# Kernel optimization log

Hardware: AMD Instinct MI355X
Metric: run time of the kernel (lower is better)

Reference implementation:

```python
import jax, jax.numpy as jnp
import numpy as np

ALPHA = 0.2          # LeakyReLU negative slope
NEG_INF = -9e15      # matches torch's -9000000000000000.0 mask value


def _gat_layer(x, adj_mask, W, a1, a2, concat):
    """One GraphAttentionLayerBatch (eval mode, dropout off).

    The original builds a_input = [h_i || h_j] of shape [B,N,N,2F] and dots
    with a = [a1; a2]; that is mathematically the separable score
    a1.h_i + a2.h_j, which we compute directly without the O(N^2*2F) tensor.
    """
    h = jnp.einsum('bnf,fo->bno', x, W)            # [B, N, F_out]
    f1 = jnp.einsum('bno,o->bn', h, a1)            # a1 . h_i
    f2 = jnp.einsum('bno,o->bn', h, a2)            # a2 . h_j
    e = jax.nn.leaky_relu(f1[:, :, None] + f2[:, None, :], negative_slope=ALPHA)
    e = jnp.where(adj_mask, e, NEG_INF)            # [B, N, N]
    att = jax.nn.softmax(e, axis=2)
    h_prime = jnp.einsum('bnm,bmo->bno', att, h)   # [B, N, F_out]
    return jax.nn.elu(h_prime) if concat else h_prime


def setup_inputs() -> dict:
    key = jax.random.key(0)
    ks = jax.random.split(key, 9)
    B, N, nfeat, nhid, nclass, H = 32, 512, 128, 64, 16, 8
    x = jax.random.normal(ks[0], (B, N, nfeat), dtype=jnp.float32)
    adj = jax.random.randint(ks[1], (B, N, N), 0, 2, dtype=jnp.int32)
    W_heads = jax.random.normal(ks[2], (H, nfeat, nhid), dtype=jnp.float32) * 0.1
    a1_heads = jax.random.normal(ks[3], (H, nhid), dtype=jnp.float32) * 0.1
    a2_heads = jax.random.normal(ks[4], (H, nhid), dtype=jnp.float32) * 0.1
    W_out = jax.random.normal(ks[5], (nhid * H, nclass), dtype=jnp.float32) * 0.05
    a1_out = jax.random.normal(ks[6], (nclass,), dtype=jnp.float32) * 0.1
    a2_out = jax.random.normal(ks[7], (nclass,), dtype=jnp.float32) * 0.1
    return {"x": x, "adj": adj, "W_heads": W_heads, "a1_heads": a1_heads,
            "a2_heads": a2_heads, "W_out": W_out, "a1_out": a1_out,
            "a2_out": a2_out}


def reference(x, adj, W_heads, a1_heads, a2_heads, W_out, a1_out, a2_out):
    mask = adj > 0  # [B, N, N]
    # multi-head attention layers (concat=True)
    heads = jax.vmap(lambda W, a1, a2: _gat_layer(x, mask, W, a1, a2, True))(
        W_heads, a1_heads, a2_heads)              # [H, B, N, nhid]
    H, B, N, F = heads.shape
    x_cat = jnp.transpose(heads, (1, 2, 0, 3)).reshape(B, N, H * F)
    # output attention layer (concat=False)
    return _gat_layer(x_cat, mask, W_out, a1_out, a2_out, False)
```

## Files before the change

### kernel.cpp

```cpp
#include <hip/hip_runtime.h>
#include <hip/hip_bf16.h>

#define GB 32
#define GN 512
#define GFIN 128
#define GFH 64
#define GH 8
#define GC 16

typedef short short8 __attribute__((ext_vector_type(8)));
typedef float f32x4 __attribute__((ext_vector_type(4)));

__device__ __forceinline__ ushort f2bf(float f) {
  unsigned u = __float_as_uint(f);
  return (ushort)((u + 0x7FFFu + ((u >> 16) & 1u)) >> 16);
}
__device__ __forceinline__ unsigned pk2(float a, float b) {
  float2 f2; f2.x = a; f2.y = b;
  __hip_bfloat162 h = __float22bfloat162_rn(f2);
  union { __hip_bfloat162 h; unsigned u; } cv;
  cv.h = h;
  return cv.u;
}
__device__ __forceinline__ short8 ones8() {
  short8 o;
#pragma unroll
  for (int i = 0; i < 8; ++i) o[i] = (short)0x3F80;
  return o;
}
__device__ __forceinline__ float fdiv_fast(float a, float b) {
  return a * __builtin_amdgcn_rcpf(b);
}

__global__ __launch_bounds__(256) void k_pack_gemm1(
    const int* __restrict__ adj, unsigned* __restrict__ mw,
    const float* __restrict__ xg, const float* __restrict__ Wg,
    const float* __restrict__ a1g, const float* __restrict__ a2g,
    ushort* __restrict__ VTg, float* __restrict__ f1g, float* __restrict__ f2g,
    const float* __restrict__ Wog, ushort* __restrict__ WoT) {
  __shared__ ushort Wt[64][136];
  __shared__ ushort xl[128][136];
  int blk = blockIdx.x;
  int tid = threadIdx.x;

  if (blk == 5120) {
    for (int i = tid; i < 512 * GC; i += 256) {
      int k = i & 511, cc = i >> 9;
      WoT[cc * 512 + k] = f2bf(Wog[(size_t)k * GC + cc]);
    }
    return;
  }
  if (blk >= 1024) {
    int pblk = blk - 1024;
    int lane = tid & 63;
    int base = pblk * 2048 + tid;
    int v[8];
#pragma unroll
    for (int it = 0; it < 8; ++it) v[it] = adj[(size_t)base + it * 256];
#pragma unroll
    for (int it = 0; it < 8; ++it) {
      unsigned long long m = __ballot(v[it] > 0);
      int idx = base + it * 256;
      if (lane == 0)       mw[idx >> 5] = (unsigned)m;
      else if (lane == 32) mw[idx >> 5] = (unsigned)(m >> 32);
    }
    return;
  }

  int bh = blk >> 2, rq = blk & 3;
  int b = bh >> 3, h = bh & 7;
  int r0 = rq * 128;
  int lane = tid & 63, w = tid >> 6;
  int c = lane & 15, q = lane >> 4;

  const float* Wh = Wg + (size_t)h * GFIN * GFH;
  for (int i = tid; i < GFIN * GFH; i += 256) {
    int f = i >> 6, j = i & 63;
    Wt[j][f] = f2bf(Wh[i]);
  }
  const float* xb = xg + ((size_t)b * GN + r0) * GFIN;
  for (int u = tid; u < 128 * 32; u += 256) {
    int row = u >> 5, c4 = u & 31;
    float4 xf = *(const float4*)&xb[(size_t)row * GFIN + c4 * 4];
    uint2 us;
    us.x = pk2(xf.x, xf.y);
    us.y = pk2(xf.z, xf.w);
    *(uint2*)&xl[row][c4 * 4] = us;
  }
  __syncthreads();

  short8 Bf[4][4];
#pragma unroll
  for (int cb = 0; cb < 4; ++cb)
#pragma unroll
    for (int kk = 0; kk < 4; ++kk)
      Bf[cb][kk] = *(const short8*)&Wt[cb * 16 + c][kk * 32 + q * 8];

  float a1v[4], a2v[4];
#pragma unroll
  for (int cb = 0; cb < 4; ++cb) {
    a1v[cb] = a1g[h * 64 + cb * 16 + c];
    a2v[cb] = a2g[h * 64 + cb * 16 + c];
  }

  f32x4 acc[2][4];
#pragma unroll
  for (int r = 0; r < 2; ++r)
#pragma unroll
    for (int cb = 0; cb < 4; ++cb) acc[r][cb] = (f32x4){0.f, 0.f, 0.f, 0.f};

#pragma unroll
  for (int kk = 0; kk < 4; ++kk) {
    short8 A0 = *(const short8*)&xl[(w * 2 + 0) * 16 + c][kk * 32 + q * 8];
    short8 A1 = *(const short8*)&xl[(w * 2 + 1) * 16 + c][kk * 32 + q * 8];
#pragma unroll
    for (int cb = 0; cb < 4; ++cb) {
      acc[0][cb] = __builtin_amdgcn_mfma_f32_16x16x32_bf16(A0, Bf[cb][kk], acc[0][cb], 0, 0, 0);
      acc[1][cb] = __builtin_amdgcn_mfma_f32_16x16x32_bf16(A1, Bf[cb][kk], acc[1][cb], 0, 0, 0);
    }
  }

  ushort* VT = VTg + (size_t)bh * GN * GFH;
  float* f1o = f1g + (size_t)bh * GN;
  float* f2o = f2g + (size_t)bh * GN;
#pragma unroll
  for (int rbi = 0; rbi < 2; ++rbi) {
    int rowb = r0 + (w * 2 + rbi) * 16 + q * 4;
    float v1[4] = {0.f, 0.f, 0.f, 0.f}, v2[4] = {0.f, 0.f, 0.f, 0.f};
#pragma unroll
    for (int cb = 0; cb < 4; ++cb) {
      f32x4 a = acc[rbi][cb];
      uint2 vs;
      vs.x = pk2(a[0], a[1]);
      vs.y = pk2(a[2], a[3]);
      *(uint2*)&VT[(size_t)(cb * 16 + c) * GN + rowb] = vs;
#pragma unroll
      for (int i = 0; i < 4; ++i) {
        v1[i] += a[i] * a1v[cb];
        v2[i] += a[i] * a2v[cb];
      }
    }
#pragma unroll
    for (int i = 0; i < 4; ++i) {
#pragma unroll
      for (int off = 1; off < 16; off <<= 1) {
        v1[i] += __shfl_xor(v1[i], off);
        v2[i] += __shfl_xor(v2[i], off);
      }
      if (c == 0) { f1o[rowb + i] = v1[i]; f2o[rowb + i] = v2[i]; }
    }
  }
}

__global__ __launch_bounds__(256, 4) void k_attn1(
    const ushort* __restrict__ VTg, const unsigned* __restrict__ mwg,
    const float* __restrict__ f1g, const float* __restrict__ f2g,
    ushort* __restrict__ xcb) {
  __shared__ ushort P[2][16][520];
  int blk = blockIdx.x;
  int bh = blk & 255, slice = blk >> 8;
  int b = bh >> 3, h = bh & 7;
  int r0 = slice * 64;
  int tid = threadIdx.x, lane = tid & 63, w = tid >> 6;
  int c = lane & 15, q = lane >> 4;

  const unsigned* mwb = mwg + (size_t)b * GN * 16;
  const float* f1w = f1g + (size_t)bh * GN;
  const float* f2w = f2g + (size_t)bh * GN;

  float4 fa = *(const float4*)&f2w[lane * 8];
  float4 fb = *(const float4*)&f2w[lane * 8 + 4];
  float E2[8], e2[8];
  {
    float f2v[8] = {fa.x, fa.y, fa.z, fa.w, fb.x, fb.y, fb.z, fb.w};
#pragma unroll
    for (int i = 0; i < 8; ++i) {
      E2[i] = __expf(f2v[i]);
      e2[i] = __expf(0.2f * f2v[i]);
    }
  }
  float f1v = f1w[r0 + lane];
  float E1v = __expf(f1v), e1v = __expf(0.2f * f1v);

  const ushort* VT = VTg + (size_t)bh * GN * GFH + (size_t)(w * 16 + c) * GN + q * 8;
  short8 Bf[16];
#pragma unroll
  for (int kk = 0; kk < 16; ++kk) Bf[kk] = *(const short8*)&VT[kk * 32];
  const short8 ONES = ones8();

  unsigned mn[4];
#pragma unroll
  for (int ri = 0; ri < 4; ++ri)
    mn[ri] = mwb[(size_t)(r0 + w + 4 * ri) * 16 + (lane >> 2)];
#pragma unroll
  for (int ri = 0; ri < 4; ++ri) {
    float E1r = __shfl(E1v, w + 4 * ri);
    float e1r = __shfl(e1v, w + 4 * ri);
    unsigned mb = (mn[ri] >> (8 * (lane & 3))) & 0xffu;
    float p[8];
#pragma unroll
    for (int i = 0; i < 8; ++i) {
      float v = fmaxf(E1r * E2[i], e1r * e2[i]);
      p[i] = ((mb >> i) & 1u) ? v : 0.f;
    }
    uint4 u;
    u.x = pk2(p[0], p[1]);
    u.y = pk2(p[2], p[3]);
    u.z = pk2(p[4], p[5]);
    u.w = pk2(p[6], p[7]);
    *(uint4*)&P[0][w + 4 * ri][lane * 8] = u;
  }
#pragma unroll
  for (int ri = 0; ri < 4; ++ri)
    mn[ri] = mwb[(size_t)(r0 + 16 + w + 4 * ri) * 16 + (lane >> 2)];
  __syncthreads();

#pragma unroll
  for (int t = 0; t < 4; ++t) {
    int tb = r0 + t * 16;
    const ushort (*Pc)[520] = P[t & 1];

    f32x4 acc = (f32x4){0.f, 0.f, 0.f, 0.f};
    f32x4 aL = (f32x4){0.f, 0.f, 0.f, 0.f};
#pragma unroll
    for (int kk = 0; kk < 16; ++kk) {
      short8 A = *(const short8*)&Pc[c][kk * 32 + q * 8];
      acc = __builtin_amdgcn_mfma_f32_16x16x32_bf16(A, Bf[kk], acc, 0, 0, 0);
      aL  = __builtin_amdgcn_mfma_f32_16x16x32_bf16(A, ONES, aL, 0, 0, 0);
    }

    if (t < 3) {
#pragma unroll
      for (int ri = 0; ri < 4; ++ri) {
        float E1r = __shfl(E1v, (t + 1) * 16 + w + 4 * ri);
        float e1r = __shfl(e1v, (t + 1) * 16 + w + 4 * ri);
        unsigned mb = (mn[ri] >> (8 * (lane & 3))) & 0xffu;
        float p[8];
#pragma unroll
        for (int i = 0; i < 8; ++i) {
          float v = fmaxf(E1r * E2[i], e1r * e2[i]);
          p[i] = ((mb >> i) & 1u) ? v : 0.f;
        }
        uint4 u;
        u.x = pk2(p[0], p[1]);
        u.y = pk2(p[2], p[3]);
        u.z = pk2(p[4], p[5]);
        u.w = pk2(p[6], p[7]);
        *(uint4*)&P[(t + 1) & 1][w + 4 * ri][lane * 8] = u;
      }
      if (t < 2) {
#pragma unroll
        for (int ri = 0; ri < 4; ++ri)
          mn[ri] = mwb[(size_t)(tb + 32 + w + 4 * ri) * 16 + (lane >> 2)];
      }
    }

#pragma unroll
    for (int i = 0; i < 4; ++i) {
      int row = tb + q * 4 + i;
      float v = fdiv_fast(acc[i], fmaxf(aL[i], 1e-30f));
      v = v > 0.f ? v : __expf(v) - 1.f;
      xcb[((size_t)(b * GN + row)) * 512 + h * 64 + w * 16 + c] = f2bf(v);
    }
    __syncthreads();
  }
}

__global__ __launch_bounds__(256) void k_gemm2(
    const ushort* __restrict__ xcb, const ushort* __restrict__ WoT,
    const float* __restrict__ a1o, const float* __restrict__ a2o,
    ushort* __restrict__ hTg, float* __restrict__ f1bg,
    float* __restrict__ f2bg) {
  int vb = blockIdx.x;
  int b = vb >> 3, r0 = (vb & 7) * 64;
  int tid = threadIdx.x, lane = tid & 63, w = tid >> 6;
  int c = lane & 15, q = lane >> 4;

  short8 Bf[16];
#pragma unroll
  for (int kk = 0; kk < 16; ++kk)
    Bf[kk] = *(const short8*)&WoT[(size_t)c * 512 + kk * 32 + q * 8];

  const ushort* xrow = xcb + ((size_t)(b * GN + r0 + w * 16 + c)) * 512 + q * 8;
  f32x4 acc = (f32x4){0.f, 0.f, 0.f, 0.f};
#pragma unroll
  for (int kk = 0; kk < 16; ++kk) {
    short8 A = *(const short8*)&xrow[kk * 32];
    acc = __builtin_amdgcn_mfma_f32_16x16x32_bf16(A, Bf[kk], acc, 0, 0, 0);
  }

  float a1v = a1o[c], a2v = a2o[c];
  int rowb = r0 + w * 16 + q * 4;
  uint2 vs;
  vs.x = pk2(acc[0], acc[1]);
  vs.y = pk2(acc[2], acc[3]);
  *(uint2*)&hTg[((size_t)b * GC + c) * 512 + rowb] = vs;
#pragma unroll
  for (int i = 0; i < 4; ++i) {
    float v1 = acc[i] * a1v, v2 = acc[i] * a2v;
#pragma unroll
    for (int off = 1; off < 16; off <<= 1) {
      v1 += __shfl_xor(v1, off);
      v2 += __shfl_xor(v2, off);
    }
    if (c == 0) {
      f1bg[(size_t)b * GN + rowb + i] = v1;
      f2bg[(size_t)b * GN + rowb + i] = v2;
    }
  }
}

__global__ __launch_bounds__(256) void k_attn2(
    const ushort* __restrict__ hTg, const unsigned* __restrict__ mwg,
    const float* __restrict__ f1g, const float* __restrict__ f2g,
    float* __restrict__ outg) {
  __shared__ ushort P[32][520];
  int vb = blockIdx.x;
  int b = vb >> 4, r0 = (vb & 15) * 32;
  int tid = threadIdx.x, lane = tid & 63, w = tid >> 6;
  int c = lane & 15, q = lane >> 4;
  const short8 ONES = ones8();

  const unsigned* mwb = mwg + (size_t)b * GN * 16;
  const float* f1w = f1g + (size_t)b * GN;
  const float* f2w = f2g + (size_t)b * GN;

  float4 fa = *(const float4*)&f2w[lane * 8];
  float4 fb = *(const float4*)&f2w[lane * 8 + 4];
  float E2[8], e2[8];
  {
    float f2v[8] = {fa.x, fa.y, fa.z, fa.w, fb.x, fb.y, fb.z, fb.w};
#pragma unroll
    for (int i = 0; i < 8; ++i) {
      E2[i] = __expf(f2v[i]);
      e2[i] = __expf(0.2f * f2v[i]);
    }
  }
  float f1v = 0.f;
  if (lane < 8) f1v = f1w[r0 + w * 8 + lane];
  float E1v = __expf(f1v), e1v = __expf(0.2f * f1v);

  unsigned mword[8];
#pragma unroll
  for (int ri = 0; ri < 8; ++ri)
    mword[ri] = mwb[(size_t)(r0 + w * 8 + ri) * 16 + (lane >> 2)];
#pragma unroll
  for (int ri = 0; ri < 8; ++ri) {
    float E1r = __shfl(E1v, ri);
    float e1r = __shfl(e1v, ri);
    unsigned mb = (mword[ri] >> (8 * (lane & 3))) & 0xffu;
    float p[8];
#pragma unroll
    for (int i = 0; i < 8; ++i) {
      float v = fmaxf(E1r * E2[i], e1r * e2[i]);
      p[i] = ((mb >> i) & 1u) ? v : 0.f;
    }
    uint4 u;
    u.x = pk2(p[0], p[1]);
    u.y = pk2(p[2], p[3]);
    u.z = pk2(p[4], p[5]);
    u.w = pk2(p[6], p[7]);
    *(uint4*)&P[w * 8 + ri][lane * 8] = u;
  }
  __syncthreads();

  if (w < 2) {
    short8 Bf[16];
#pragma unroll
    for (int kk = 0; kk < 16; ++kk)
      Bf[kk] = *(const short8*)&hTg[((size_t)b * GC + c) * 512 + kk * 32 + q * 8];
    f32x4 acc = (f32x4){0.f, 0.f, 0.f, 0.f};
    f32x4 aL = (f32x4){0.f, 0.f, 0.f, 0.f};
#pragma unroll
    for (int kk = 0; kk < 16; ++kk) {
      short8 A = *(const short8*)&P[w * 16 + c][kk * 32 + q * 8];
      acc = __builtin_amdgcn_mfma_f32_16x16x32_bf16(A, Bf[kk], acc, 0, 0, 0);
      aL  = __builtin_amdgcn_mfma_f32_16x16x32_bf16(A, ONES, aL, 0, 0, 0);
    }
#pragma unroll
    for (int i = 0; i < 4; ++i) {
      int row = r0 + w * 16 + q * 4 + i;
      outg[((size_t)(b * GN + row)) * GC + c] =
          fdiv_fast(acc[i], fmaxf(aL[i], 1e-30f));
    }
  }
}

extern "C" void kernel_launch(void* const* d_in, const int* in_sizes, int n_in,
                              void* d_out, int out_size, void* d_ws, size_t ws_size,
                              hipStream_t stream) {
  (void)in_sizes; (void)n_in; (void)out_size;
  const float* x   = (const float*)d_in[0];
  const int*   adj = (const int*)d_in[1];
  const float* Whd = (const float*)d_in[2];
  const float* a1h = (const float*)d_in[3];
  const float* a2h = (const float*)d_in[4];
  const float* Wo  = (const float*)d_in[5];
  const float* a1o = (const float*)d_in[6];
  const float* a2o = (const float*)d_in[7];

  size_t off = 0;
  char* base = (char*)d_ws;
  unsigned* mw = (unsigned*)(base + off); off += (size_t)GB * GN * 16 * 4;
  ushort* VT   = (ushort*)(base + off);   off += (size_t)GB * GH * GN * GFH * 2;
  ushort* xcb  = (ushort*)(base + off);   off += (size_t)GB * GN * 512 * 2;
  ushort* WoT  = (ushort*)(base + off);   off += (size_t)GC * 512 * 2;
  ushort* hT   = (ushort*)(base + off);   off += (size_t)GB * GC * GN * 2;
  float* f1    = (float*)(base + off);    off += (size_t)GB * GH * GN * 4;
  float* f2    = (float*)(base + off);    off += (size_t)GB * GH * GN * 4;
  float* f1b   = (float*)(base + off);    off += (size_t)GB * GN * 4;
  float* f2b   = (float*)(base + off);    off += (size_t)GB * GN * 4;

  if (ws_size < off) return;

  hipLaunchKernelGGL(k_pack_gemm1, dim3(5121), dim3(256), 0, stream,
                     adj, mw, x, Whd, a1h, a2h, VT, f1, f2, Wo, WoT);
  hipLaunchKernelGGL(k_attn1, dim3(2048), dim3(256), 0, stream,
                     VT, mw, f1, f2, xcb);
  hipLaunchKernelGGL(k_gemm2, dim3(256), dim3(256), 0, stream,
                     xcb, WoT, a1o, a2o, hT, f1b, f2b);
  hipLaunchKernelGGL(k_attn2, dim3(512), dim3(256), 0, stream,
                     hT, mw, f1b, f2b, (float*)d_out);
}
```

Baseline: 150.5 us.

## Fuse adjacency mask packing into first attention kernel, reading int adj directly

```diff
diff --git a/kernel.cpp b/kernel.cpp
--- a/kernel.cpp
+++ b/kernel.cpp
@@ -32,8 +32,7 @@
   return a * __builtin_amdgcn_rcpf(b);
 }
 
-__global__ __launch_bounds__(256) void k_pack_gemm1(
-    const int* __restrict__ adj, unsigned* __restrict__ mw,
+__global__ __launch_bounds__(256) void k_gemm1(
     const float* __restrict__ xg, const float* __restrict__ Wg,
     const float* __restrict__ a1g, const float* __restrict__ a2g,
     ushort* __restrict__ VTg, float* __restrict__ f1g, float* __restrict__ f2g,
@@ -43,26 +42,10 @@
   int blk = blockIdx.x;
   int tid = threadIdx.x;
 
-  if (blk == 5120) {
+  if (blk == 1024) {
     for (int i = tid; i < 512 * GC; i += 256) {
       int k = i & 511, cc = i >> 9;
       WoT[cc * 512 + k] = f2bf(Wog[(size_t)k * GC + cc]);
-    }
-    return;
-  }
-  if (blk >= 1024) {
-    int pblk = blk - 1024;
-    int lane = tid & 63;
-    int base = pblk * 2048 + tid;
-    int v[8];
-#pragma unroll
-    for (int it = 0; it < 8; ++it) v[it] = adj[(size_t)base + it * 256];
-#pragma unroll
-    for (int it = 0; it < 8; ++it) {
-      unsigned long long m = __ballot(v[it] > 0);
-      int idx = base + it * 256;
-      if (lane == 0)       mw[idx >> 5] = (unsigned)m;
-      else if (lane == 32) mw[idx >> 5] = (unsigned)(m >> 32);
     }
     return;
   }
@@ -153,18 +136,20 @@
 }
 
 __global__ __launch_bounds__(256, 4) void k_attn1(
-    const ushort* __restrict__ VTg, const unsigned* __restrict__ mwg,
+    const ushort* __restrict__ VTg, const int* __restrict__ adj,
     const float* __restrict__ f1g, const float* __restrict__ f2g,
-    ushort* __restrict__ xcb) {
+    ushort* __restrict__ xcb, unsigned char* __restrict__ maskb) {
   __shared__ ushort P[2][16][520];
   int blk = blockIdx.x;
-  int bh = blk & 255, slice = blk >> 8;
-  int b = bh >> 3, h = bh & 7;
+  int h = blk >> 8;
+  int rem = blk & 255;
+  int b = rem >> 3, slice = rem & 7;
+  int bh = b * 8 + h;
   int r0 = slice * 64;
   int tid = threadIdx.x, lane = tid & 63, w = tid >> 6;
   int c = lane & 15, q = lane >> 4;
 
-  const unsigned* mwb = mwg + (size_t)b * GN * 16;
+  const int* adjb = adj + (size_t)b * GN * GN;
   const float* f1w = f1g + (size_t)bh * GN;
   const float* f2w = f2g + (size_t)bh * GN;
 
@@ -188,20 +173,30 @@
   for (int kk = 0; kk < 16; ++kk) Bf[kk] = *(const short8*)&VT[kk * 32];
   const short8 ONES = ones8();
 
-  unsigned mn[4];
-#pragma unroll
-  for (int ri = 0; ri < 4; ++ri)
-    mn[ri] = mwb[(size_t)(r0 + w + 4 * ri) * 16 + (lane >> 2)];
+  int4 av[4][2];
+#pragma unroll
+  for (int ri = 0; ri < 4; ++ri) {
+    const int* ar = adjb + (size_t)(r0 + w + 4 * ri) * GN + lane * 8;
+    av[ri][0] = *(const int4*)ar;
+    av[ri][1] = *(const int4*)(ar + 4);
+  }
 #pragma unroll
   for (int ri = 0; ri < 4; ++ri) {
     float E1r = __shfl(E1v, w + 4 * ri);
     float e1r = __shfl(e1v, w + 4 * ri);
-    unsigned mb = (mn[ri] >> (8 * (lane & 3))) & 0xffu;
+    int4 a0 = av[ri][0], a1 = av[ri][1];
+    int m[8] = {a0.x, a0.y, a0.z, a0.w, a1.x, a1.y, a1.z, a1.w};
     float p[8];
 #pragma unroll
     for (int i = 0; i < 8; ++i) {
       float v = fmaxf(E1r * E2[i], e1r * e2[i]);
-      p[i] = ((mb >> i) & 1u) ? v : 0.f;
+      p[i] = (m[i] > 0) ? v : 0.f;
+    }
+    if (h == 0) {
+      unsigned mb = (unsigned)(m[0] > 0);
+#pragma unroll
+      for (int i = 1; i < 8; ++i) mb |= ((unsigned)(m[i] > 0)) << i;
+      maskb[((size_t)b * GN + r0 + w + 4 * ri) * 64 + lane] = (unsigned char)mb;
     }
     uint4 u;
     u.x = pk2(p[0], p[1]);
@@ -211,8 +206,11 @@
     *(uint4*)&P[0][w + 4 * ri][lane * 8] = u;
   }
 #pragma unroll
-  for (int ri = 0; ri < 4; ++ri)
-    mn[ri] = mwb[(size_t)(r0 + 16 + w + 4 * ri) * 16 + (lane >> 2)];
+  for (int ri = 0; ri < 4; ++ri) {
+    const int* ar = adjb + (size_t)(r0 + 16 + w + 4 * ri) * GN + lane * 8;
+    av[ri][0] = *(const int4*)ar;
+    av[ri][1] = *(const int4*)(ar + 4);
+  }
   __syncthreads();
 
 #pragma unroll
@@ -234,12 +232,20 @@
       for (int ri = 0; ri < 4; ++ri) {
         float E1r = __shfl(E1v, (t + 1) * 16 + w + 4 * ri);
         float e1r = __shfl(e1v, (t + 1) * 16 + w + 4 * ri);
-        unsigned mb = (mn[ri] >> (8 * (lane & 3))) & 0xffu;
+        int4 a0 = av[ri][0], a1 = av[ri][1];
+        int m[8] = {a0.x, a0.y, a0.z, a0.w, a1.x, a1.y, a1.z, a1.w};
         float p[8];
 #pragma unroll
         for (int i = 0; i < 8; ++i) {
           float v = fmaxf(E1r * E2[i], e1r * e2[i]);
-          p[i] = ((mb >> i) & 1u) ? v : 0.f;
+          p[i] = (m[i] > 0) ? v : 0.f;
+        }
+        if (h == 0) {
+          unsigned mb = (unsigned)(m[0] > 0);
+#pragma unroll
+          for (int i = 1; i < 8; ++i) mb |= ((unsigned)(m[i] > 0)) << i;
+          maskb[((size_t)b * GN + tb + 16 + w + 4 * ri) * 64 + lane] =
+              (unsigned char)mb;
         }
         uint4 u;
         u.x = pk2(p[0], p[1]);
@@ -250,8 +256,11 @@
       }
       if (t < 2) {
 #pragma unroll
-        for (int ri = 0; ri < 4; ++ri)
-          mn[ri] = mwb[(size_t)(tb + 32 + w + 4 * ri) * 16 + (lane >> 2)];
+        for (int ri = 0; ri < 4; ++ri) {
+          const int* ar = adjb + (size_t)(tb + 32 + w + 4 * ri) * GN + lane * 8;
+          av[ri][0] = *(const int4*)ar;
+          av[ri][1] = *(const int4*)(ar + 4);
+        }
       }
     }
 
@@ -311,7 +320,7 @@
 }
 
 __global__ __launch_bounds__(256) void k_attn2(
-    const ushort* __restrict__ hTg, const unsigned* __restrict__ mwg,
+    const ushort* __restrict__ hTg, const unsigned char* __restrict__ maskb,
     const float* __restrict__ f1g, const float* __restrict__ f2g,
     float* __restrict__ outg) {
   __shared__ ushort P[32][520];
@@ -321,7 +330,6 @@
   int c = lane & 15, q = lane >> 4;
   const short8 ONES = ones8();
 
-  const unsigned* mwb = mwg + (size_t)b * GN * 16;
   const float* f1w = f1g + (size_t)b * GN;
   const float* f2w = f2g + (size_t)b * GN;
 
@@ -343,12 +351,12 @@
   unsigned mword[8];
 #pragma unroll
   for (int ri = 0; ri < 8; ++ri)
-    mword[ri] = mwb[(size_t)(r0 + w * 8 + ri) * 16 + (lane >> 2)];
+    mword[ri] = maskb[((size_t)b * GN + r0 + w * 8 + ri) * 64 + lane];
 #pragma unroll
   for (int ri = 0; ri < 8; ++ri) {
     float E1r = __shfl(E1v, ri);
     float e1r = __shfl(e1v, ri);
-    unsigned mb = (mword[ri] >> (8 * (lane & 3))) & 0xffu;
+    unsigned mb = mword[ri];
     float p[8];
 #pragma unroll
     for (int i = 0; i < 8; ++i) {
@@ -401,7 +409,7 @@
 
   size_t off = 0;
   char* base = (char*)d_ws;
-  unsigned* mw = (unsigned*)(base + off); off += (size_t)GB * GN * 16 * 4;
+  unsigned char* mb = (unsigned char*)(base + off); off += (size_t)GB * GN * 64;
   ushort* VT   = (ushort*)(base + off);   off += (size_t)GB * GH * GN * GFH * 2;
   ushort* xcb  = (ushort*)(base + off);   off += (size_t)GB * GN * 512 * 2;
   ushort* WoT  = (ushort*)(base + off);   off += (size_t)GC * 512 * 2;
@@ -413,12 +421,12 @@
 
   if (ws_size < off) return;
 
-  hipLaunchKernelGGL(k_pack_gemm1, dim3(5121), dim3(256), 0, stream,
-                     adj, mw, x, Whd, a1h, a2h, VT, f1, f2, Wo, WoT);
+  hipLaunchKernelGGL(k_gemm1, dim3(1025), dim3(256), 0, stream,
+                     x, Whd, a1h, a2h, VT, f1, f2, Wo, WoT);
   hipLaunchKernelGGL(k_attn1, dim3(2048), dim3(256), 0, stream,
-                     VT, mw, f1, f2, xcb);
+                     VT, adj, f1, f2, xcb, mb);
   hipLaunchKernelGGL(k_gemm2, dim3(256), dim3(256), 0, stream,
                      xcb, WoT, a1o, a2o, hT, f1b, f2b);
   hipLaunchKernelGGL(k_attn2, dim3(512), dim3(256), 0, stream,
-                     hT, mw, f1b, f2b, (float*)d_out);
-}
+                     hT, mb, f1b, f2b, (float*)d_out);
+}
```

Result: slower. 190.6 us (+26.7%).
